# Optimization experiments

Hardware: AMD Instinct MI355X
Metric: run time of the kernel (lower is better)

The kernel has to match this reference:

```python
import jax, jax.numpy as jnp
import numpy as np

B, D, H, W_ = 2, 256, 64, 64


def setup_inputs() -> dict:
    key = jax.random.key(0)
    k1, k2 = jax.random.split(key)
    x = jax.random.normal(k1, (B, D, H, W_), dtype=jnp.float32)
    W = jax.random.normal(k2, (3 * D, D), dtype=jnp.float32) * 0.02  # 1x1 conv weight [out,in]
    b = jnp.zeros((3 * D,), dtype=jnp.float32)
    return {"x": x, "W": W, "b": b}


def reference(x, W, b):
    Bs, d, h, w = x.shape
    N = h * w
    sqrtV = d ** 0.25  # sqrt(sqrt(d)); q,k each divided -> qk^T / sqrt(d)
    # 1x1 conv == per-pixel linear over channels
    qkv = jnp.einsum('bchw,oc->bohw', x, W) + b[None, :, None, None]
    q, k, v = jnp.split(qkv, 3, axis=1)
    q = q.reshape(Bs, d, N).transpose(0, 2, 1) / sqrtV  # [B,N,d]
    k = k.reshape(Bs, d, N).transpose(0, 2, 1) / sqrtV
    v = v.reshape(Bs, d, N).transpose(0, 2, 1)
    # Sinkhorn (eps=1, max_iter=1, uniform marginals 1/N), log domain.
    # cost C = -q k^T  =>  -C = q k^T (softmax-style logits)
    negC = jnp.einsum('bnd,bmd->bnm', q, k)  # [B,N,N]
    logm = jnp.log(1.0 / N + 1e-8).astype(x.dtype)
    u = logm - jax.nn.logsumexp(negC, axis=-1)            # [B,N] row update
    vpot = logm - jax.nn.logsumexp(negC + u[..., None], axis=-2)  # [B,N] col update
    pi = jnp.exp(negC + u[..., None] + vpot[:, None, :])  # transport plan = attn
    out = jnp.einsum('bnm,bmd->bnd', pi, v)               # [B,N,d]
    return out.transpose(0, 2, 1).reshape(Bs, d, h, w)
```

## Files before the change

kernel.cpp:

```cpp
#include <hip/hip_runtime.h>
#include <hip/hip_bf16.h>
#include <math.h>

typedef __bf16 bf16;
typedef __bf16 bf16x8 __attribute__((ext_vector_type(8)));
typedef __bf16 bf16x4 __attribute__((ext_vector_type(4)));
typedef float floatx4 __attribute__((ext_vector_type(4)));

#define NPIX 4096
#define DCH 256
#define LSTR 72

#define OFF_XB   ((size_t)0)
#define OFF_WB   ((size_t)4194304)
#define OFF_Q    ((size_t)4587520)
#define OFF_K    ((size_t)8781824)
#define OFF_V    ((size_t)12976128)
#define OFF_E    ((size_t)17170432)
#define OFF_VPP  ((size_t)84279296)
#define OFF_PART ((size_t)88473600)
#define OFF_RS   ((size_t)122028032)
#define OFF_CS   ((size_t)122060800)

__global__ __launch_bounds__(256) void transpose_x(
    const float* __restrict__ x, bf16* __restrict__ xb)
{
  __shared__ float ts[64][65];
  const int t = threadIdx.x;
  const int b = blockIdx.z, n0 = blockIdx.x * 64, c0 = blockIdx.y * 64;
  const float* xp = x + ((size_t)b * DCH + c0) * NPIX + n0;
  for (int i = 0; i < 4; i++) {
    int slot = t + i * 256;
    int c = slot >> 4, nq = (slot & 15) * 4;
    float4 v = *(const float4*)(xp + (size_t)c * NPIX + nq);
    ts[c][nq + 0] = v.x; ts[c][nq + 1] = v.y; ts[c][nq + 2] = v.z; ts[c][nq + 3] = v.w;
  }
  __syncthreads();
  for (int i = 0; i < 2; i++) {
    int slot = t + i * 256;
    int n = slot >> 3, cq = (slot & 7) * 8;
    bf16x8 pk;
    for (int j = 0; j < 8; j++) pk[j] = (bf16)ts[cq + j][n];
    *(bf16x8*)(xb + ((size_t)b * NPIX + n0 + n) * DCH + c0 + cq) = pk;
  }
}

__global__ __launch_bounds__(256) void convert_w(
    const float* __restrict__ W, bf16* __restrict__ wb)
{
  size_t i = ((size_t)blockIdx.x * 256 + threadIdx.x) * 4;
  float4 v = *(const float4*)(W + i);
  bf16x4 pk = { (bf16)v.x, (bf16)v.y, (bf16)v.z, (bf16)v.w };
  *(bf16x4*)(wb + i) = pk;
}

__global__ __launch_bounds__(256) void conv_mfma(
    const bf16* __restrict__ xb, const bf16* __restrict__ wb,
    const float* __restrict__ bias,
    bf16* __restrict__ qb, bf16* __restrict__ kb, bf16* __restrict__ vb)
{
  __shared__ bf16 at[128 * LSTR];
  __shared__ bf16 bt[128 * LSTR];
  __shared__ float bs[128];
  const int t  = threadIdx.x;
  const int n0 = blockIdx.x * 128;
  const int o0 = blockIdx.y * 128;
  if (t < 128) bs[t] = bias[o0 + t];
  const int lane = t & 63, wave = t >> 6;
  const int wm = wave >> 1, wn = wave & 1;
  const int l15 = lane & 15, quad = lane >> 4;

  floatx4 acc[4][4];
  for (int i=0;i<4;i++) for (int j=0;j<4;j++) for (int r=0;r<4;r++) acc[i][j][r] = 0.f;

  for (int k0 = 0; k0 < DCH; k0 += 64) {
    for (int i = 0; i < 4; i++) {
      int slot = t + i*256; int row = slot >> 3, ch = slot & 7;
      *(bf16x8*)&at[row*LSTR + ch*8] = *(const bf16x8*)(wb + (size_t)(o0+row)*DCH + k0 + ch*8);
    }
    for (int i = 0; i < 4; i++) {
      int slot = t + i*256; int row = slot >> 3, ch = slot & 7;
      *(bf16x8*)&bt[row*LSTR + ch*8] = *(const bf16x8*)(xb + (size_t)(n0+row)*DCH + k0 + ch*8);
    }
    __syncthreads();
    for (int kk = 0; kk < 2; kk++) {
      bf16x8 af[4], bfr[4];
      for (int f = 0; f < 4; f++)
        af[f]  = *(const bf16x8*)&at[(wm*64 + f*16 + l15)*LSTR + kk*32 + quad*8];
      for (int f = 0; f < 4; f++)
        bfr[f] = *(const bf16x8*)&bt[(wn*64 + f*16 + l15)*LSTR + kk*32 + quad*8];
      for (int fm = 0; fm < 4; fm++)
        for (int fn = 0; fn < 4; fn++)
          acc[fm][fn] = __builtin_amdgcn_mfma_f32_16x16x32_bf16(af[fm], bfr[fn], acc[fm][fn], 0, 0, 0);
    }
    __syncthreads();
  }

  const float scale = (o0 < 512) ? 0.25f : 1.0f;
  bf16* dst; int od;
  if (o0 < 256)      { dst = qb; od = o0; }
  else if (o0 < 512) { dst = kb; od = o0 - 256; }
  else               { dst = vb; od = o0 - 512; }

  for (int fm = 0; fm < 4; fm++)
    for (int fn = 0; fn < 4; fn++) {
      int o_l = wm*64 + fm*16 + quad*4;
      int n_g = n0 + wn*64 + fn*16 + l15;
      bf16x4 pk;
      for (int r = 0; r < 4; r++)
        pk[r] = (bf16)((acc[fm][fn][r] + bs[o_l + r]) * scale);
      *(bf16x4*)(dst + (size_t)n_g * DCH + od + o_l) = pk;
    }
}

__global__ __launch_bounds__(256) void pass_a(
    const bf16* __restrict__ qb, const bf16* __restrict__ kb,
    bf16* __restrict__ E, float* __restrict__ rowsum)
{
  __shared__ bf16 kt[128 * LSTR];
  __shared__ bf16 qt[128 * LSTR];
  __shared__ float rowpart[128];
  const int b = blockIdx.z;
  qb += (size_t)b * NPIX * DCH;
  kb += (size_t)b * NPIX * DCH;
  E  += (size_t)b * NPIX * NPIX;
  rowsum += b * NPIX;
  const int t  = threadIdx.x;
  const int m0 = blockIdx.x * 128;
  const int n0 = blockIdx.y * 128;
  const int lane = t & 63, wave = t >> 6;
  const int wm = wave >> 1, wn = wave & 1;
  const int l15 = lane & 15, quad = lane >> 4;

  floatx4 acc[4][4];
  for (int i=0;i<4;i++) for (int j=0;j<4;j++) for (int r=0;r<4;r++) acc[i][j][r] = 0.f;

  for (int k0 = 0; k0 < DCH; k0 += 64) {
    for (int i = 0; i < 4; i++) {
      int slot = t + i*256; int row = slot >> 3, ch = slot & 7;
      *(bf16x8*)&kt[row*LSTR + ch*8] = *(const bf16x8*)(kb + (size_t)(m0+row)*DCH + k0 + ch*8);
    }
    for (int i = 0; i < 4; i++) {
      int slot = t + i*256; int row = slot >> 3, ch = slot & 7;
      *(bf16x8*)&qt[row*LSTR + ch*8] = *(const bf16x8*)(qb + (size_t)(n0+row)*DCH + k0 + ch*8);
    }
    __syncthreads();
    for (int kk = 0; kk < 2; kk++) {
      bf16x8 af[4], bfr[4];
      for (int f = 0; f < 4; f++)
        af[f]  = *(const bf16x8*)&kt[(wm*64 + f*16 + l15)*LSTR + kk*32 + quad*8];
      for (int f = 0; f < 4; f++)
        bfr[f] = *(const bf16x8*)&qt[(wn*64 + f*16 + l15)*LSTR + kk*32 + quad*8];
      for (int fm = 0; fm < 4; fm++)
        for (int fn = 0; fn < 4; fn++)
          acc[fm][fn] = __builtin_amdgcn_mfma_f32_16x16x32_bf16(af[fm], bfr[fn], acc[fm][fn], 0, 0, 0);
    }
    __syncthreads();
  }

  if (t < 128) rowpart[t] = 0.f;
  __syncthreads();

  float rsum[4] = {0.f, 0.f, 0.f, 0.f};
  for (int fm = 0; fm < 4; fm++)
    for (int fn = 0; fn < 4; fn++) {
      int n_g = n0 + wn*64 + fn*16 + l15;
      int m_g = m0 + wm*64 + fm*16 + quad*4;
      bf16x4 pk;
      float s = 0.f;
      for (int r = 0; r < 4; r++) {
        float e = __expf(acc[fm][fn][r]);
        pk[r] = (bf16)e;
        s += e;
      }
      *(bf16x4*)(E + (size_t)n_g * NPIX + m_g) = pk;
      rsum[fn] += s;
    }
  for (int fn = 0; fn < 4; fn++) {
    float s = rsum[fn];
    s += __shfl_xor(s, 16);
    s += __shfl_xor(s, 32);
    if (quad == 0) atomicAdd(&rowpart[wn*64 + fn*16 + l15], s);
  }
  __syncthreads();
  if (t < 128) atomicAdd(&rowsum[n0 + t], rowpart[t]);
}

__global__ __launch_bounds__(256) void col_pass(
    const bf16* __restrict__ E, const float* __restrict__ rowsum,
    float* __restrict__ colsum, float logm)
{
  __shared__ float eus[32];
  const int b = blockIdx.z;
  E += (size_t)b * NPIX * NPIX;
  rowsum += b * NPIX;
  colsum += b * NPIX;
  const int t = threadIdx.x;
  const int col = blockIdx.x * 1024 + t * 4;
  const int nbase = blockIdx.y * 32;
  if (t < 32) eus[t] = __expf(logm - __logf(rowsum[nbase + t]));
  __syncthreads();
  float acc[4] = {0.f, 0.f, 0.f, 0.f};
  for (int r = 0; r < 32; r++) {
    float eu = eus[r];
    bf16x4 ev = *(const bf16x4*)(E + (size_t)(nbase + r) * NPIX + col);
    for (int i = 0; i < 4; i++) acc[i] += eu * (float)ev[i];
  }
  for (int i = 0; i < 4; i++) atomicAdd(&colsum[col + i], acc[i]);
}

__global__ __launch_bounds__(256) void vpp_kernel(
    const bf16* __restrict__ vb, const float* __restrict__ colsum,
    bf16* __restrict__ vppT, float logm)
{
  __shared__ float ts[64][65];
  __shared__ float ef[64];
  const int b = blockIdx.z;
  vb += (size_t)b * NPIX * DCH;
  colsum += b * NPIX;
  vppT += (size_t)b * DCH * NPIX;
  const int t = threadIdx.x;
  const int m0 = blockIdx.x * 64, d0 = blockIdx.y * 64;
  if (t < 64) ef[t] = __expf(logm - __logf(colsum[m0 + t]));
  __syncthreads();
  for (int i = 0; i < 2; i++) {
    int slot = t + i * 256;
    int m = slot >> 3, dq = (slot & 7) * 8;
    bf16x8 v = *(const bf16x8*)(vb + (size_t)(m0 + m) * DCH + d0 + dq);
    float s = ef[m];
    for (int j = 0; j < 8; j++) ts[dq + j][m] = s * (float)v[j];
  }
  __syncthreads();
  for (int i = 0; i < 2; i++) {
    int slot = t + i * 256;
    int d = slot >> 3, mq = (slot & 7) * 8;
    bf16x8 pk;
    for (int j = 0; j < 8; j++) pk[j] = (bf16)ts[d][mq + j];
    *(bf16x8*)(vppT + (size_t)(d0 + d) * NPIX + m0 + mq) = pk;
  }
}

__global__ __launch_bounds__(256) void pass_c(
    const bf16* __restrict__ E, const bf16* __restrict__ vppT,
    const float* __restrict__ rowsum, float* __restrict__ part, float logm)
{
  __shared__ bf16 et[128 * LSTR];
  __shared__ bf16 vt[128 * LSTR];
  __shared__ float eus[128];
  const int z = blockIdx.z;
  const int b = z >> 2, kc = z & 3;
  E += (size_t)b * NPIX * NPIX;
  vppT += (size_t)b * DCH * NPIX;
  rowsum += b * NPIX;
  part += (size_t)(b * 4 + kc) * DCH * NPIX;
  const int t  = threadIdx.x;
  const int n0 = blockIdx.x * 128;
  const int d0 = blockIdx.y * 128;
  const int mstart = kc * 1024;
  if (t < 128) eus[t] = __expf(logm - __logf(rowsum[n0 + t]));
  const int lane = t & 63, wave = t >> 6;
  const int wn = wave >> 1, wd = wave & 1;
  const int l15 = lane & 15, quad = lane >> 4;

  floatx4 acc[4][4];
  for (int i=0;i<4;i++) for (int j=0;j<4;j++) for (int r=0;r<4;r++) acc[i][j][r] = 0.f;
  __syncthreads();

  for (int k0 = mstart; k0 < mstart + 1024; k0 += 64) {
    for (int i = 0; i < 4; i++) {
      int slot = t + i*256; int row = slot >> 3, ch = slot & 7;
      *(bf16x8*)&et[row*LSTR + ch*8] = *(const bf16x8*)(E + (size_t)(n0+row)*NPIX + k0 + ch*8);
    }
    for (int i = 0; i < 4; i++) {
      int slot = t + i*256; int row = slot >> 3, ch = slot & 7;
      *(bf16x8*)&vt[row*LSTR + ch*8] = *(const bf16x8*)(vppT + (size_t)(d0+row)*NPIX + k0 + ch*8);
    }
    __syncthreads();
    for (int kk = 0; kk < 2; kk++) {
      bf16x8 af[4], bfr[4];
      for (int f = 0; f < 4; f++)
        af[f]  = *(const bf16x8*)&et[(wn*64 + f*16 + l15)*LSTR + kk*32 + quad*8];
      for (int f = 0; f < 4; f++)
        bfr[f] = *(const bf16x8*)&vt[(wd*64 + f*16 + l15)*LSTR + kk*32 + quad*8];
      for (int fn = 0; fn < 4; fn++)
        for (int fd = 0; fd < 4; fd++)
          acc[fn][fd] = __builtin_amdgcn_mfma_f32_16x16x32_bf16(af[fn], bfr[fd], acc[fn][fd], 0, 0, 0);
    }
    __syncthreads();
  }

  for (int fn = 0; fn < 4; fn++)
    for (int fd = 0; fd < 4; fd++) {
      int d_g = d0 + wd*64 + fd*16 + l15;
      int n_l = wn*64 + fn*16 + quad*4;
      float4 o;
      o.x = acc[fn][fd][0] * eus[n_l + 0];
      o.y = acc[fn][fd][1] * eus[n_l + 1];
      o.z = acc[fn][fd][2] * eus[n_l + 2];
      o.w = acc[fn][fd][3] * eus[n_l + 3];
      *(float4*)(part + (size_t)d_g * NPIX + n0 + n_l) = o;
    }
}

__global__ __launch_bounds__(256) void reduce_k(
    const float* __restrict__ part, float* __restrict__ outp)
{
  size_t i4 = ((size_t)blockIdx.x * 256 + threadIdx.x) * 4;
  size_t b = i4 >> 20;
  size_t off = i4 & (size_t)1048575;
  const float* p = part + b * 4 * (size_t)1048576 + off;
  float4 a = *(const float4*)(p);
  float4 bq = *(const float4*)(p + (size_t)1048576);
  float4 c = *(const float4*)(p + (size_t)2097152);
  float4 d = *(const float4*)(p + (size_t)3145728);
  float4 s = { a.x+bq.x+c.x+d.x, a.y+bq.y+c.y+d.y, a.z+bq.z+c.z+d.z, a.w+bq.w+c.w+d.w };
  *(float4*)(outp + i4) = s;
}

extern "C" void kernel_launch(void* const* d_in, const int* in_sizes, int n_in,
                              void* d_out, int out_size, void* d_ws, size_t ws_size,
                              hipStream_t stream) {
  (void)in_sizes; (void)n_in; (void)out_size; (void)ws_size;
  const float* x    = (const float*)d_in[0];
  const float* Wm   = (const float*)d_in[1];
  const float* bias = (const float*)d_in[2];
  float* outp = (float*)d_out;
  char* ws = (char*)d_ws;

  bf16*  xb   = (bf16*)(ws + OFF_XB);
  bf16*  wb   = (bf16*)(ws + OFF_WB);
  bf16*  qb   = (bf16*)(ws + OFF_Q);
  bf16*  kb   = (bf16*)(ws + OFF_K);
  bf16*  vb   = (bf16*)(ws + OFF_V);
  bf16*  E    = (bf16*)(ws + OFF_E);
  bf16*  vppT = (bf16*)(ws + OFF_VPP);
  float* part = (float*)(ws + OFF_PART);
  float* rs   = (float*)(ws + OFF_RS);
  float* cs   = (float*)(ws + OFF_CS);

  const float logm = logf(1.0f / 4096.0f + 1e-8f);

  hipMemsetAsync(ws + OFF_RS, 0, 65536, stream);

  transpose_x<<<dim3(64, 4, 2), 256, 0, stream>>>(x, xb);
  convert_w<<<192, 256, 0, stream>>>(Wm, wb);
  conv_mfma<<<dim3(64, 6), 256, 0, stream>>>(xb, wb, bias, qb, kb, vb);

  pass_a<<<dim3(32, 32, 2), 256, 0, stream>>>(qb, kb, E, rs);
  col_pass<<<dim3(4, 128, 2), 256, 0, stream>>>(E, rs, cs, logm);
  vpp_kernel<<<dim3(64, 4, 2), 256, 0, stream>>>(vb, cs, vppT, logm);
  pass_c<<<dim3(32, 2, 8), 256, 0, stream>>>(E, vppT, rs, part, logm);
  reduce_k<<<2048, 256, 0, stream>>>(part, outp);
}
```

Measured before the change: 183.6 us.

## Stage GEMM tiles via direct global-to-LDS loads with XOR-swizzled layout

Replaces the register-staged global→LDS copies in the conv, pass_a and pass_c GEMM kernels with global_load_lds direct transfers of 16 bytes per lane. The padded LDS stride is dropped for an unpadded 64-column layout, and bank conflicts are avoided with an XOR swizzle applied on the global source addresses and the fragment reads. The aim is to cut VGPR traffic and instruction count on tile staging and to shrink LDS use. It relies on the wave-contiguous LDS write pattern of the builtin matching the swizzle, and there is still no double buffering.

```diff
diff --git a/kernel.cpp b/kernel.cpp
--- a/kernel.cpp
+++ b/kernel.cpp
@@ -6,6 +6,9 @@
 typedef __bf16 bf16x8 __attribute__((ext_vector_type(8)));
 typedef __bf16 bf16x4 __attribute__((ext_vector_type(4)));
 typedef float floatx4 __attribute__((ext_vector_type(4)));
+
+typedef const __attribute__((address_space(1))) void* gas_t;
+typedef __attribute__((address_space(3))) void* las_t;
 
 #define NPIX 4096
 #define DCH 256
@@ -22,6 +25,19 @@
 #define OFF_RS   ((size_t)122028032)
 #define OFF_CS   ((size_t)122060800)
 
+__device__ __forceinline__ void stage_tile(const bf16* __restrict__ g0, size_t rstride,
+                                           bf16* lds, int t) {
+  const int wbase = (t >> 6) << 6;
+#pragma unroll
+  for (int i = 0; i < 4; i++) {
+    int slot = i * 256 + t;
+    int row = slot >> 3, seg = slot & 7;
+    const bf16* g = g0 + (size_t)row * rstride + ((seg ^ (row & 7)) << 3);
+    bf16* l = lds + (size_t)(i * 256 + wbase) * 8;
+    __builtin_amdgcn_global_load_lds((gas_t)g, (las_t)l, 16, 0, 0);
+  }
+}
+
 __global__ __launch_bounds__(256) void transpose_x(
     const float* __restrict__ x, bf16* __restrict__ xb)
 {
@@ -59,8 +75,8 @@
     const float* __restrict__ bias,
     bf16* __restrict__ qb, bf16* __restrict__ kb, bf16* __restrict__ vb)
 {
-  __shared__ bf16 at[128 * LSTR];
-  __shared__ bf16 bt[128 * LSTR];
+  __shared__ bf16 at[128 * 64];
+  __shared__ bf16 bt[128 * 64];
   __shared__ float bs[128];
   const int t  = threadIdx.x;
   const int n0 = blockIdx.x * 128;
@@ -69,26 +85,22 @@
   const int lane = t & 63, wave = t >> 6;
   const int wm = wave >> 1, wn = wave & 1;
   const int l15 = lane & 15, quad = lane >> 4;
+  const int l7 = l15 & 7;
 
   floatx4 acc[4][4];
   for (int i=0;i<4;i++) for (int j=0;j<4;j++) for (int r=0;r<4;r++) acc[i][j][r] = 0.f;
 
   for (int k0 = 0; k0 < DCH; k0 += 64) {
-    for (int i = 0; i < 4; i++) {
-      int slot = t + i*256; int row = slot >> 3, ch = slot & 7;
-      *(bf16x8*)&at[row*LSTR + ch*8] = *(const bf16x8*)(wb + (size_t)(o0+row)*DCH + k0 + ch*8);
-    }
-    for (int i = 0; i < 4; i++) {
-      int slot = t + i*256; int row = slot >> 3, ch = slot & 7;
-      *(bf16x8*)&bt[row*LSTR + ch*8] = *(const bf16x8*)(xb + (size_t)(n0+row)*DCH + k0 + ch*8);
-    }
+    stage_tile(wb + (size_t)o0 * DCH + k0, DCH, at, t);
+    stage_tile(xb + (size_t)n0 * DCH + k0, DCH, bt, t);
     __syncthreads();
     for (int kk = 0; kk < 2; kk++) {
       bf16x8 af[4], bfr[4];
-      for (int f = 0; f < 4; f++)
-        af[f]  = *(const bf16x8*)&at[(wm*64 + f*16 + l15)*LSTR + kk*32 + quad*8];
-      for (int f = 0; f < 4; f++)
-        bfr[f] = *(const bf16x8*)&bt[(wn*64 + f*16 + l15)*LSTR + kk*32 + quad*8];
+      int sw = ((kk * 4 + quad) ^ l7) * 8;
+      for (int f = 0; f < 4; f++)
+        af[f]  = *(const bf16x8*)&at[(wm*64 + f*16 + l15)*64 + sw];
+      for (int f = 0; f < 4; f++)
+        bfr[f] = *(const bf16x8*)&bt[(wn*64 + f*16 + l15)*64 + sw];
       for (int fm = 0; fm < 4; fm++)
         for (int fn = 0; fn < 4; fn++)
           acc[fm][fn] = __builtin_amdgcn_mfma_f32_16x16x32_bf16(af[fm], bfr[fn], acc[fm][fn], 0, 0, 0);
@@ -117,8 +129,8 @@
     const bf16* __restrict__ qb, const bf16* __restrict__ kb,
     bf16* __restrict__ E, float* __restrict__ rowsum)
 {
-  __shared__ bf16 kt[128 * LSTR];
-  __shared__ bf16 qt[128 * LSTR];
+  __shared__ bf16 kt[128 * 64];
+  __shared__ bf16 qt[128 * 64];
   __shared__ float rowpart[128];
   const int b = blockIdx.z;
   qb += (size_t)b * NPIX * DCH;
@@ -131,26 +143,22 @@
   const int lane = t & 63, wave = t >> 6;
   const int wm = wave >> 1, wn = wave & 1;
   const int l15 = lane & 15, quad = lane >> 4;
+  const int l7 = l15 & 7;
 
   floatx4 acc[4][4];
   for (int i=0;i<4;i++) for (int j=0;j<4;j++) for (int r=0;r<4;r++) acc[i][j][r] = 0.f;
 
   for (int k0 = 0; k0 < DCH; k0 += 64) {
-    for (int i = 0; i < 4; i++) {
-      int slot = t + i*256; int row = slot >> 3, ch = slot & 7;
-      *(bf16x8*)&kt[row*LSTR + ch*8] = *(const bf16x8*)(kb + (size_t)(m0+row)*DCH + k0 + ch*8);
-    }
-    for (int i = 0; i < 4; i++) {
-      int slot = t + i*256; int row = slot >> 3, ch = slot & 7;
-      *(bf16x8*)&qt[row*LSTR + ch*8] = *(const bf16x8*)(qb + (size_t)(n0+row)*DCH + k0 + ch*8);
-    }
+    stage_tile(kb + (size_t)m0 * DCH + k0, DCH, kt, t);
+    stage_tile(qb + (size_t)n0 * DCH + k0, DCH, qt, t);
     __syncthreads();
     for (int kk = 0; kk < 2; kk++) {
       bf16x8 af[4], bfr[4];
-      for (int f = 0; f < 4; f++)
-        af[f]  = *(const bf16x8*)&kt[(wm*64 + f*16 + l15)*LSTR + kk*32 + quad*8];
-      for (int f = 0; f < 4; f++)
-        bfr[f] = *(const bf16x8*)&qt[(wn*64 + f*16 + l15)*LSTR + kk*32 + quad*8];
+      int sw = ((kk * 4 + quad) ^ l7) * 8;
+      for (int f = 0; f < 4; f++)
+        af[f]  = *(const bf16x8*)&kt[(wm*64 + f*16 + l15)*64 + sw];
+      for (int f = 0; f < 4; f++)
+        bfr[f] = *(const bf16x8*)&qt[(wn*64 + f*16 + l15)*64 + sw];
       for (int fm = 0; fm < 4; fm++)
         for (int fn = 0; fn < 4; fn++)
           acc[fm][fn] = __builtin_amdgcn_mfma_f32_16x16x32_bf16(af[fm], bfr[fn], acc[fm][fn], 0, 0, 0);
@@ -244,8 +252,8 @@
     const bf16* __restrict__ E, const bf16* __restrict__ vppT,
     const float* __restrict__ rowsum, float* __restrict__ part, float logm)
 {
-  __shared__ bf16 et[128 * LSTR];
-  __shared__ bf16 vt[128 * LSTR];
+  __shared__ bf16 et[128 * 64];
+  __shared__ bf16 vt[128 * 64];
   __shared__ float eus[128];
   const int z = blockIdx.z;
   const int b = z >> 2, kc = z & 3;
@@ -261,27 +269,23 @@
   const int lane = t & 63, wave = t >> 6;
   const int wn = wave >> 1, wd = wave & 1;
   const int l15 = lane & 15, quad = lane >> 4;
+  const int l7 = l15 & 7;
 
   floatx4 acc[4][4];
   for (int i=0;i<4;i++) for (int j=0;j<4;j++) for (int r=0;r<4;r++) acc[i][j][r] = 0.f;
   __syncthreads();
 
   for (int k0 = mstart; k0 < mstart + 1024; k0 += 64) {
-    for (int i = 0; i < 4; i++) {
-      int slot = t + i*256; int row = slot >> 3, ch = slot & 7;
-      *(bf16x8*)&et[row*LSTR + ch*8] = *(const bf16x8*)(E + (size_t)(n0+row)*NPIX + k0 + ch*8);
-    }
-    for (int i = 0; i < 4; i++) {
-      int slot = t + i*256; int row = slot >> 3, ch = slot & 7;
-      *(bf16x8*)&vt[row*LSTR + ch*8] = *(const bf16x8*)(vppT + (size_t)(d0+row)*NPIX + k0 + ch*8);
-    }
+    stage_tile(E + (size_t)n0 * NPIX + k0, NPIX, et, t);
+    stage_tile(vppT + (size_t)d0 * NPIX + k0, NPIX, vt, t);
     __syncthreads();
     for (int kk = 0; kk < 2; kk++) {
       bf16x8 af[4], bfr[4];
-      for (int f = 0; f < 4; f++)
-        af[f]  = *(const bf16x8*)&et[(wn*64 + f*16 + l15)*LSTR + kk*32 + quad*8];
-      for (int f = 0; f < 4; f++)
-        bfr[f] = *(const bf16x8*)&vt[(wd*64 + f*16 + l15)*LSTR + kk*32 + quad*8];
+      int sw = ((kk * 4 + quad) ^ l7) * 8;
+      for (int f = 0; f < 4; f++)
+        af[f]  = *(const bf16x8*)&et[(wn*64 + f*16 + l15)*64 + sw];
+      for (int f = 0; f < 4; f++)
+        bfr[f] = *(const bf16x8*)&vt[(wd*64 + f*16 + l15)*64 + sw];
       for (int fn = 0; fn < 4; fn++)
         for (int fd = 0; fd < 4; fd++)
           acc[fn][fd] = __builtin_amdgcn_mfma_f32_16x16x32_bf16(af[fn], bfr[fd], acc[fn][fd], 0, 0, 0);
```

Result: no change. 186.4 us (+1.5%).
